# Kernel tuning notes

Hardware: AMD Instinct MI355X
Metric: run time of the kernel (lower is better)

## Reference

```python
import jax, jax.numpy as jnp
import numpy as np

NUM_USERS = 100000
NUM_ITEMS = 50000
N = NUM_USERS + NUM_ITEMS
EMB = 64
N_LAYERS = 3
N_EDGES = 4800000
BATCH = 4096


def setup_inputs() -> dict:
    key = jax.random.key(0)
    ks = jax.random.split(key, 8)
    users = jax.random.randint(ks[0], (BATCH,), 0, NUM_USERS, dtype=jnp.int64 if jax.config.jax_enable_x64 else jnp.int32)
    pos_items = jax.random.randint(ks[1], (BATCH,), 0, NUM_ITEMS)
    neg_items = jax.random.randint(ks[2], (BATCH,), 0, NUM_ITEMS)
    adj_rows = jax.random.randint(ks[3], (N_EDGES,), 0, N)
    adj_cols = jax.random.randint(ks[4], (N_EDGES,), 0, N)
    # scale values like a degree-normalized adjacency (~1/deg) to keep magnitudes stable
    adj_vals = jax.random.uniform(ks[5], (N_EDGES,), dtype=jnp.float32) * (1.0 / 32.0)
    user_emb = jax.random.normal(ks[6], (NUM_USERS, EMB), dtype=jnp.float32) * 0.1
    item_emb = jax.random.normal(ks[7], (NUM_ITEMS, EMB), dtype=jnp.float32) * 0.1
    return {"users": users, "pos_items": pos_items, "neg_items": neg_items,
            "adj_rows": adj_rows, "adj_cols": adj_cols, "adj_vals": adj_vals,
            "user_emb": user_emb, "item_emb": item_emb}


def _spmm(rows, cols, vals, x):
    # sparse (N,N) @ dense (N,E): gather columns, scale, scatter-add to rows
    gathered = x[cols] * vals[:, None]          # [n_edges, EMB]
    return jax.ops.segment_sum(gathered, rows, num_segments=N)


def reference(users, pos_items, neg_items, adj_rows, adj_cols, adj_vals, user_emb, item_emb):
    emb = jnp.concatenate([user_emb, item_emb], axis=0)  # [N, EMB]
    acc = emb
    cur = emb
    for _ in range(N_LAYERS):
        cur = _spmm(adj_rows, adj_cols, adj_vals, cur)
        acc = acc + cur
    final = acc / (N_LAYERS + 1)                # layer-wise mean
    users_emb = final[:NUM_USERS]
    items_emb = final[NUM_USERS:]
    u = users_emb[users]                        # [B, EMB]
    pos = items_emb[pos_items]
    neg = items_emb[neg_items]
    pos_scores = jnp.sum(u * pos, axis=1)       # [B]
    neg_scores = jnp.sum(u * neg, axis=1)
    return (pos_scores, neg_scores)
```

## Files before the change

### kernel.cpp

```cpp
#include <hip/hip_runtime.h>

#define NUM_USERS 100000
#define NUM_ITEMS 50000
#define NNODES    150000
#define EMB       64
#define NEDGES    4800000
#define BATCH     4096
#define BUCKETS   293
#define BROWS     512
#define EPB       8192
#define NBLK_A    586
#define CAP       17408
#define NSAMP     (3 * BATCH)

typedef unsigned short u16;
typedef unsigned int   u32;

__device__ inline float bf2f(u16 u) { return __uint_as_float(((u32)u) << 16); }
__device__ inline u16 f2bf(float f) {
    u32 b = __float_as_uint(f);
    b += 0x7FFFu + ((b >> 16) & 1u);
    return (u16)(b >> 16);
}
__device__ inline u32 pack2(float a, float b) {
    return (u32)f2bf(a) | ((u32)f2bf(b) << 16);
}

__global__ void init_kernel(const float* __restrict__ user_emb,
                            const float* __restrict__ item_emb,
                            u16* __restrict__ l0) {
    long i = (long)blockIdx.x * blockDim.x + threadIdx.x;
    const long n4 = (long)NNODES * EMB / 4;
    if (i >= n4) return;
    const long nu4 = (long)NUM_USERS * EMB / 4;
    float4 v = (i < nu4) ? ((const float4*)user_emb)[i]
                         : ((const float4*)item_emb)[i - nu4];
    ushort4 o;
    o.x = f2bf(v.x); o.y = f2bf(v.y); o.z = f2bf(v.z); o.w = f2bf(v.w);
    ((ushort4*)l0)[i] = o;
}

__global__ void __launch_bounds__(512) binA_kernel(const int* __restrict__ rows,
                                                   const int* __restrict__ cols,
                                                   const float* __restrict__ vals,
                                                   int* __restrict__ bfill,
                                                   int2* __restrict__ tmp) {
    __shared__ int2 ebuf[EPB];
    __shared__ int  hist[BUCKETS];
    __shared__ int  start[BUCKETS];
    __shared__ int  cursor[BUCKETS];
    __shared__ int  gbase[BUCKETS];
    const int tid = threadIdx.x;
    for (int i = tid; i < BUCKETS; i += 512) hist[i] = 0;
    __syncthreads();

    const long base = (long)blockIdx.x * EPB;
    int rsave[16];
    #pragma unroll
    for (int k = 0; k < 16; ++k) {
        long e = base + (long)k * 512 + tid;
        int r = -1;
        if (e < NEDGES) {
            r = rows[e];
            atomicAdd(&hist[r >> 9], 1);
        }
        rsave[k] = r;
    }
    __syncthreads();

    if (tid < 64) {
        int carry = 0;
        for (int cb = 0; cb < BUCKETS; cb += 64) {
            int i = cb + tid;
            int orig = (i < BUCKETS) ? hist[i] : 0;
            int x = orig;
            #pragma unroll
            for (int d = 1; d < 64; d <<= 1) {
                int t = __shfl_up(x, d, 64);
                if (tid >= d) x += t;
            }
            int total = __shfl(x, 63, 64);
            if (i < BUCKETS) { start[i] = x - orig + carry; cursor[i] = x - orig + carry; }
            carry += total;
        }
    }
    __syncthreads();

    for (int b = tid; b < BUCKETS; b += 512) {
        int h = hist[b];
        gbase[b] = h ? b * CAP + atomicAdd(&bfill[b], h) : 0;
    }

    #pragma unroll
    for (int k = 0; k < 16; ++k) {
        int r = rsave[k];
        if (r >= 0) {
            long e = base + (long)k * 512 + tid;
            int pos = atomicAdd(&cursor[r >> 9], 1);
            ebuf[pos] = make_int2(((r & 511) << 18) | cols[e], __float_as_int(vals[e]));
        }
    }
    __syncthreads();

    const int wv = tid >> 6, lane = tid & 63;
    const int* eb32 = (const int*)ebuf;
    int* gtmp = (int*)tmp;
    for (int b = wv; b < BUCKETS; b += 8) {
        int cnt2 = hist[b] * 2;
        if (!cnt2) continue;
        int  s2 = start[b] * 2;
        long d2 = (long)gbase[b] * 2;
        for (int i = lane; i < cnt2; i += 64)
            gtmp[d2 + i] = eb32[s2 + i];
    }
}

__global__ void scan_buckets(const int* __restrict__ bfill, int* __restrict__ bucketBase) {
    int lane = threadIdx.x;
    int carry = 0;
    for (int cb = 0; cb < BUCKETS; cb += 64) {
        int i = cb + lane;
        int orig = (i < BUCKETS) ? bfill[i] : 0;
        int x = orig;
        #pragma unroll
        for (int d = 1; d < 64; d <<= 1) {
            int t = __shfl_up(x, d, 64);
            if (lane >= d) x += t;
        }
        int total = __shfl(x, 63, 64);
        if (i < BUCKETS) bucketBase[i] = x - orig + carry;
        carry += total;
    }
}

__global__ void __launch_bounds__(512) binB_kernel(const int* __restrict__ bfill,
                                                   const int* __restrict__ bucketBase,
                                                   const int2* __restrict__ tmp,
                                                   int* __restrict__ rowPtr,
                                                   int2* __restrict__ csr) {
    const int bucket = blockIdx.x;
    __shared__ int lhist[BROWS];
    __shared__ int rp[BROWS];
    __shared__ int fill[BROWS];
    const int t = threadIdx.x;
    lhist[t] = 0; fill[t] = 0;
    __syncthreads();

    const int cnt = bfill[bucket];
    const int2* src = tmp + (long)bucket * CAP;
    for (int k = t; k < cnt; k += 512)
        atomicAdd(&lhist[src[k].x >> 18], 1);
    __syncthreads();

    const int gb = bucketBase[bucket];
    if (t < 64) {
        int carry = 0;
        for (int cb = 0; cb < BROWS; cb += 64) {
            int i = cb + t;
            int orig = lhist[i];
            int x = orig;
            #pragma unroll
            for (int d = 1; d < 64; d <<= 1) {
                int tt = __shfl_up(x, d, 64);
                if (t >= d) x += tt;
            }
            int total = __shfl(x, 63, 64);
            rp[i] = x - orig + carry + gb;
            carry += total;
        }
    }
    __syncthreads();

    int rowIdx = bucket * BROWS + t;
    rowPtr[rowIdx] = rp[t];

    for (int k = t; k < cnt; k += 512) {
        int2 p = src[k];
        int rL = p.x >> 18;
        int pos = rp[rL] + atomicAdd(&fill[rL], 1);
        csr[pos] = make_int2(p.x & 0x3FFFF, p.y);
    }
}

#define ACCX(V, X) { \
    a[0] += (V) * __uint_as_float((X).x << 16); \
    a[1] += (V) * __uint_as_float((X).x & 0xFFFF0000u); \
    a[2] += (V) * __uint_as_float((X).y << 16); \
    a[3] += (V) * __uint_as_float((X).y & 0xFFFF0000u); \
    a[4] += (V) * __uint_as_float((X).z << 16); \
    a[5] += (V) * __uint_as_float((X).z & 0xFFFF0000u); \
    a[6] += (V) * __uint_as_float((X).w << 16); \
    a[7] += (V) * __uint_as_float((X).w & 0xFFFF0000u); }

__global__ void spmm_csr(const int* __restrict__ rowPtr, const int2* __restrict__ csr,
                         const u16* __restrict__ cur, u16* __restrict__ nxt) {
    int gtid = blockIdx.x * blockDim.x + threadIdx.x;
    int row = gtid >> 3;
    int t   = gtid & 7;
    if (row >= NNODES) return;
    int beg = rowPtr[row], end = rowPtr[row + 1];
    float a[8];
    #pragma unroll
    for (int i = 0; i < 8; ++i) a[i] = 0.f;

    int e = beg;
    for (; e + 7 < end; e += 8) {
        int2 p[8];
        #pragma unroll
        for (int j = 0; j < 8; ++j) p[j] = csr[e + j];
        uint4 x[8];
        #pragma unroll
        for (int j = 0; j < 8; ++j)
            x[j] = *(const uint4*)(cur + ((long)p[j].x << 6) + (t << 3));
        #pragma unroll
        for (int j = 0; j < 8; ++j) {
            float v = __int_as_float(p[j].y);
            ACCX(v, x[j]);
        }
    }
    for (; e < end; ++e) {
        int2 p = csr[e];
        float v = __int_as_float(p.y);
        uint4 x = *(const uint4*)(cur + ((long)p.x << 6) + (t << 3));
        ACCX(v, x);
    }

    uint4 o;
    o.x = pack2(a[0], a[1]);
    o.y = pack2(a[2], a[3]);
    o.z = pack2(a[4], a[5]);
    o.w = pack2(a[6], a[7]);
    *(uint4*)(nxt + ((long)row << 6) + (t << 3)) = o;
}

__global__ void spmm_sampled(const int* __restrict__ users,
                             const int* __restrict__ pos_items,
                             const int* __restrict__ neg_items,
                             const int* __restrict__ rowPtr, const int2* __restrict__ csr,
                             const u16* __restrict__ cur, float* __restrict__ sampled) {
    int gtid = blockIdx.x * blockDim.x + threadIdx.x;
    int slot = gtid >> 3;
    int t    = gtid & 7;
    if (slot >= NSAMP) return;
    int row;
    if (slot < BATCH)          row = users[slot];
    else if (slot < 2 * BATCH) row = pos_items[slot - BATCH] + NUM_USERS;
    else                       row = neg_items[slot - 2 * BATCH] + NUM_USERS;

    int beg = rowPtr[row], end = rowPtr[row + 1];
    float a[8];
    #pragma unroll
    for (int i = 0; i < 8; ++i) a[i] = 0.f;

    int e = beg;
    for (; e + 7 < end; e += 8) {
        int2 p[8];
        #pragma unroll
        for (int j = 0; j < 8; ++j) p[j] = csr[e + j];
        uint4 x[8];
        #pragma unroll
        for (int j = 0; j < 8; ++j)
            x[j] = *(const uint4*)(cur + ((long)p[j].x << 6) + (t << 3));
        #pragma unroll
        for (int j = 0; j < 8; ++j) {
            float v = __int_as_float(p[j].y);
            ACCX(v, x[j]);
        }
    }
    for (; e < end; ++e) {
        int2 p = csr[e];
        float v = __int_as_float(p.y);
        uint4 x = *(const uint4*)(cur + ((long)p.x << 6) + (t << 3));
        ACCX(v, x);
    }

    float4* dst = (float4*)(sampled + ((long)slot << 6) + (t << 3));
    dst[0] = make_float4(a[0], a[1], a[2], a[3]);
    dst[1] = make_float4(a[4], a[5], a[6], a[7]);
}

__global__ void score_kernel(const int* __restrict__ users,
                             const int* __restrict__ pos_items,
                             const int* __restrict__ neg_items,
                             const float* __restrict__ uemb,
                             const float* __restrict__ iemb,
                             const u16* __restrict__ l1,
                             const u16* __restrict__ l2,
                             const float* __restrict__ sampled,
                             float* __restrict__ out) {
    int gtid = blockIdx.x * blockDim.x + threadIdx.x;
    int wave = gtid >> 6;
    int lane = threadIdx.x & 63;
    if (wave >= BATCH) return;
    int u = users[wave];
    int p = pos_items[wave];
    int n = neg_items[wave];
    long U = (long)u * EMB + lane;
    long P = (long)(p + NUM_USERS) * EMB + lane;
    long N = (long)(n + NUM_USERS) * EMB + lane;
    float ue = uemb[(long)u * EMB + lane] + bf2f(l1[U]) + bf2f(l2[U])
             + sampled[(long)wave * EMB + lane];
    float pe = iemb[(long)p * EMB + lane] + bf2f(l1[P]) + bf2f(l2[P])
             + sampled[(long)(BATCH + wave) * EMB + lane];
    float ne = iemb[(long)n * EMB + lane] + bf2f(l1[N]) + bf2f(l2[N])
             + sampled[(long)(2 * BATCH + wave) * EMB + lane];
    float ps = ue * pe;
    float ns = ue * ne;
    #pragma unroll
    for (int off = 32; off > 0; off >>= 1) {
        ps += __shfl_down(ps, off, 64);
        ns += __shfl_down(ns, off, 64);
    }
    if (lane == 0) {
        out[wave]         = ps * 0.0625f;
        out[BATCH + wave] = ns * 0.0625f;
    }
}

extern "C" void kernel_launch(void* const* d_in, const int* in_sizes, int n_in,
                              void* d_out, int out_size, void* d_ws, size_t ws_size,
                              hipStream_t stream) {
    const int*   users = (const int*)d_in[0];
    const int*   pos   = (const int*)d_in[1];
    const int*   neg   = (const int*)d_in[2];
    const int*   rows  = (const int*)d_in[3];
    const int*   cols  = (const int*)d_in[4];
    const float* vals  = (const float*)d_in[5];
    const float* uemb  = (const float*)d_in[6];
    const float* iemb  = (const float*)d_in[7];
    float* out = (float*)d_out;

    const size_t tblElems = (size_t)NNODES * EMB;
    u16*  B0      = (u16*)d_ws;
    u16*  B1      = B0 + tblElems;
    u16*  B2      = B1 + tblElems;
    int2* tmp     = (int2*)(B2 + tblElems);
    int2* csr     = (int2*)(tmp + (size_t)BUCKETS * CAP);
    int*  rowPtr  = (int*)(csr + NEDGES);
    int*  bfill   = rowPtr + 150016;
    int*  bucketB = bfill + 320;
    float* sampled= (float*)(bucketB + 320);

    hipMemsetAsync(bfill, 0, 320 * sizeof(int), stream);

    binA_kernel<<<NBLK_A, 512, 0, stream>>>(rows, cols, vals, bfill, tmp);
    scan_buckets<<<1, 64, 0, stream>>>(bfill, bucketB);
    binB_kernel<<<BUCKETS, 512, 0, stream>>>(bfill, bucketB, tmp, rowPtr, csr);

    const long n4 = (long)tblElems / 4;
    init_kernel<<<(int)((n4 + 255) / 256), 256, 0, stream>>>(uemb, iemb, B0);

    const long nth = (long)NNODES * 8;
    const int  spmmGrid = (int)((nth + 255) / 256);
    spmm_csr<<<spmmGrid, 256, 0, stream>>>(rowPtr, csr, B0, B1);
    spmm_csr<<<spmmGrid, 256, 0, stream>>>(rowPtr, csr, B1, B2);
    spmm_sampled<<<(NSAMP * 8 + 255) / 256, 256, 0, stream>>>(users, pos, neg,
                                                              rowPtr, csr, B2, sampled);

    score_kernel<<<(BATCH * 64) / 256, 256, 0, stream>>>(users, pos, neg,
                                                         uemb, iemb, B1, B2, sampled, out);
}
```

Before: 456.5 us.

## Fuse init into binning pass, drop bucket scan kernel, widen binB blocks

The bf16 embedding conversion now runs as extra blocks of the binA launch, so it overlaps with edge binning instead of being a separate launch. The separate bucket-scan kernel is removed; binB computes its global base with a per-block reduction over preceding bucket counts. binB now uses 1024 threads and keeps its edges in registers, so tmp is read once instead of twice. spmm_csr gets launch bounds asking for 8 blocks per CU. Costs are more register pressure in binB and a redundant prefix sum in every block.

```diff
diff --git a/kernel.cpp b/kernel.cpp
--- a/kernel.cpp
+++ b/kernel.cpp
@@ -11,6 +11,7 @@
 #define EPB       8192
 #define NBLK_A    586
 #define CAP       17408
+#define INIT_BLKS 2344
 #define NSAMP     (3 * BATCH)
 
 typedef unsigned short u16;
@@ -26,10 +27,9 @@
     return (u32)f2bf(a) | ((u32)f2bf(b) << 16);
 }
 
-__global__ void init_kernel(const float* __restrict__ user_emb,
-                            const float* __restrict__ item_emb,
-                            u16* __restrict__ l0) {
-    long i = (long)blockIdx.x * blockDim.x + threadIdx.x;
+__device__ inline void init_body(const float* __restrict__ user_emb,
+                                 const float* __restrict__ item_emb,
+                                 u16* __restrict__ l0, long i) {
     const long n4 = (long)NNODES * EMB / 4;
     if (i >= n4) return;
     const long nu4 = (long)NUM_USERS * EMB / 4;
@@ -44,7 +44,17 @@
                                                    const int* __restrict__ cols,
                                                    const float* __restrict__ vals,
                                                    int* __restrict__ bfill,
-                                                   int2* __restrict__ tmp) {
+                                                   int2* __restrict__ tmp,
+                                                   const float* __restrict__ uemb,
+                                                   const float* __restrict__ iemb,
+                                                   u16* __restrict__ l0) {
+    if (blockIdx.x >= NBLK_A) {
+        long ib = blockIdx.x - NBLK_A;
+        long i = ib * 1024 + threadIdx.x;
+        init_body(uemb, iemb, l0, i);
+        init_body(uemb, iemb, l0, i + 512);
+        return;
+    }
     __shared__ int2 ebuf[EPB];
     __shared__ int  hist[BUCKETS];
     __shared__ int  start[BUCKETS];
@@ -115,70 +125,70 @@
     }
 }
 
-__global__ void scan_buckets(const int* __restrict__ bfill, int* __restrict__ bucketBase) {
-    int lane = threadIdx.x;
-    int carry = 0;
-    for (int cb = 0; cb < BUCKETS; cb += 64) {
-        int i = cb + lane;
-        int orig = (i < BUCKETS) ? bfill[i] : 0;
-        int x = orig;
-        #pragma unroll
-        for (int d = 1; d < 64; d <<= 1) {
-            int t = __shfl_up(x, d, 64);
-            if (lane >= d) x += t;
-        }
-        int total = __shfl(x, 63, 64);
-        if (i < BUCKETS) bucketBase[i] = x - orig + carry;
-        carry += total;
-    }
-}
-
-__global__ void __launch_bounds__(512) binB_kernel(const int* __restrict__ bfill,
-                                                   const int* __restrict__ bucketBase,
-                                                   const int2* __restrict__ tmp,
-                                                   int* __restrict__ rowPtr,
-                                                   int2* __restrict__ csr) {
+__global__ void __launch_bounds__(1024) binB_kernel(const int* __restrict__ bfill,
+                                                    const int2* __restrict__ tmp,
+                                                    int* __restrict__ rowPtr,
+                                                    int2* __restrict__ csr) {
     const int bucket = blockIdx.x;
     __shared__ int lhist[BROWS];
     __shared__ int rp[BROWS];
     __shared__ int fill[BROWS];
+    __shared__ int gbS;
     const int t = threadIdx.x;
-    lhist[t] = 0; fill[t] = 0;
+    if (t < BROWS) { lhist[t] = 0; fill[t] = 0; }
     __syncthreads();
 
     const int cnt = bfill[bucket];
     const int2* src = tmp + (long)bucket * CAP;
-    for (int k = t; k < cnt; k += 512)
-        atomicAdd(&lhist[src[k].x >> 18], 1);
-    __syncthreads();
-
-    const int gb = bucketBase[bucket];
-    if (t < 64) {
+    int2 es[17];
+    #pragma unroll
+    for (int k = 0; k < 17; ++k) {
+        int idx = k * 1024 + t;
+        if (idx < cnt) {
+            es[k] = src[idx];
+            atomicAdd(&lhist[es[k].x >> 18], 1);
+        } else {
+            es[k].x = -1;
+        }
+    }
+    __syncthreads();
+
+    const int w = t >> 6, lane = t & 63;
+    if (w == 0) {
         int carry = 0;
         for (int cb = 0; cb < BROWS; cb += 64) {
-            int i = cb + t;
+            int i = cb + lane;
             int orig = lhist[i];
             int x = orig;
             #pragma unroll
             for (int d = 1; d < 64; d <<= 1) {
                 int tt = __shfl_up(x, d, 64);
-                if (t >= d) x += tt;
+                if (lane >= d) x += tt;
             }
             int total = __shfl(x, 63, 64);
-            rp[i] = x - orig + carry + gb;
+            rp[i] = x - orig + carry;
             carry += total;
         }
-    }
-    __syncthreads();
-
-    int rowIdx = bucket * BROWS + t;
-    rowPtr[rowIdx] = rp[t];
-
-    for (int k = t; k < cnt; k += 512) {
-        int2 p = src[k];
-        int rL = p.x >> 18;
-        int pos = rp[rL] + atomicAdd(&fill[rL], 1);
-        csr[pos] = make_int2(p.x & 0x3FFFF, p.y);
+    } else if (w == 1) {
+        int s = 0;
+        for (int i = lane; i < bucket; i += 64) s += bfill[i];
+        #pragma unroll
+        for (int off = 32; off > 0; off >>= 1) s += __shfl_down(s, off, 64);
+        if (lane == 0) gbS = s;
+    }
+    __syncthreads();
+    const int gb = gbS;
+
+    if (t < BROWS) rowPtr[bucket * BROWS + t] = gb + rp[t];
+
+    #pragma unroll
+    for (int k = 0; k < 17; ++k) {
+        int px = es[k].x;
+        if (px >= 0) {
+            int rL = px >> 18;
+            int pos = gb + rp[rL] + atomicAdd(&fill[rL], 1);
+            csr[pos] = make_int2(px & 0x3FFFF, es[k].y);
+        }
     }
 }
 
@@ -192,8 +202,9 @@
     a[6] += (V) * __uint_as_float((X).w << 16); \
     a[7] += (V) * __uint_as_float((X).w & 0xFFFF0000u); }
 
-__global__ void spmm_csr(const int* __restrict__ rowPtr, const int2* __restrict__ csr,
-                         const u16* __restrict__ cur, u16* __restrict__ nxt) {
+__global__ void __launch_bounds__(256, 8)
+spmm_csr(const int* __restrict__ rowPtr, const int2* __restrict__ csr,
+         const u16* __restrict__ cur, u16* __restrict__ nxt) {
     int gtid = blockIdx.x * blockDim.x + threadIdx.x;
     int row = gtid >> 3;
     int t   = gtid & 7;
@@ -338,17 +349,13 @@
     int2* csr     = (int2*)(tmp + (size_t)BUCKETS * CAP);
     int*  rowPtr  = (int*)(csr + NEDGES);
     int*  bfill   = rowPtr + 150016;
-    int*  bucketB = bfill + 320;
-    float* sampled= (float*)(bucketB + 320);
+    float* sampled= (float*)(bfill + 320);
 
     hipMemsetAsync(bfill, 0, 320 * sizeof(int), stream);
 
-    binA_kernel<<<NBLK_A, 512, 0, stream>>>(rows, cols, vals, bfill, tmp);
-    scan_buckets<<<1, 64, 0, stream>>>(bfill, bucketB);
-    binB_kernel<<<BUCKETS, 512, 0, stream>>>(bfill, bucketB, tmp, rowPtr, csr);
-
-    const long n4 = (long)tblElems / 4;
-    init_kernel<<<(int)((n4 + 255) / 256), 256, 0, stream>>>(uemb, iemb, B0);
+    binA_kernel<<<NBLK_A + INIT_BLKS, 512, 0, stream>>>(rows, cols, vals, bfill, tmp,
+                                                        uemb, iemb, B0);
+    binB_kernel<<<BUCKETS, 1024, 0, stream>>>(bfill, tmp, rowPtr, csr);
 
     const long nth = (long)NNODES * 8;
     const int  spmmGrid = (int)((nth + 255) / 256);
```

Measured after the change: 580.2 us. 1.27x slower.
